# Kernel tuning notes

Measured on AMD Instinct MI355X. Metric: run time of the kernel, lower is better.

The kernel has to match this reference:

```python
import jax, jax.numpy as jnp
import numpy as np

B, MD, N = 8, 256, 4096          # batch, model_dim, n_points
H, F, S = 8, 16, 32              # heads, in_feature_dim, tensor_size (3D lattice S^3)
EPS = 1e-5


def _bn(x, g, b):
    # training-mode BatchNorm1d over (batch, points), x: [B, C, N]
    m = x.mean(axis=(0, 2), keepdims=True)
    v = x.var(axis=(0, 2), keepdims=True)
    return (x - m) * jax.lax.rsqrt(v + EPS) * g[None, :, None] + b[None, :, None]


def setup_inputs() -> dict:
    key = jax.random.key(0)
    ks = jax.random.split(key, 10)
    return {
        "x": jax.random.normal(ks[0], (B, MD, N), jnp.float32),
        "pcd": jax.random.uniform(ks[1], (B, 3, N), jnp.float32, -1.0, 1.0),
        "W_kv": jax.random.normal(ks[2], (H * (F + 3), MD), jnp.float32) / np.float32(np.sqrt(MD)),
        "key_gamma": 0.1 * jax.random.normal(ks[3], (H * 3,), jnp.float32),
        "key_beta": jnp.zeros((H * 3,), jnp.float32),
        "val_gamma": jnp.ones((H * F,), jnp.float32) + 0.1 * jax.random.normal(ks[4], (H * F,), jnp.float32),
        "val_beta": jnp.zeros((H * F,), jnp.float32),
        "R": jnp.tile(jnp.eye(3, dtype=jnp.float32), (H, 1, 1)) + 0.05 * jax.random.normal(ks[5], (H, 3, 3), jnp.float32),
        "t": 0.05 * jax.random.normal(ks[6], (H, 3), jnp.float32),
        "conv_w": jax.random.normal(ks[7], (H * F, F, 3, 3, 3), jnp.float32) / np.float32(np.sqrt(F * 27)),
        "conv_b": jnp.zeros((H * F,), jnp.float32),
        "after_gamma": jnp.ones((H * F,), jnp.float32),
        "after_beta": jnp.zeros((H * F,), jnp.float32),
    }


# precomputed 8 trilinear corner offsets
_OFFS = np.array([[dx, dy, dz] for dx in (0, 1) for dy in (0, 1) for dz in (0, 1)])
_OFF_FLAT = jnp.asarray((_OFFS[:, 0] * S + _OFFS[:, 1]) * S + _OFFS[:, 2], jnp.int32)  # [8]
_OFF_BOOL = jnp.asarray(_OFFS.astype(bool))  # [8, 3]


def _forward(x, pcd, W_kv, key_gamma, key_beta, val_gamma, val_beta, R, t,
             conv_w, conv_b, after_gamma, after_beta):
    # keys/values prediction (1x1 conv == matmul)
    kv = jnp.einsum('om,bmn->bon', W_kv, x)                      # [B, H*(F+3), N]
    keys_res = _bn(kv[:, :H * 3], key_gamma, key_beta).reshape(B, H, 3, N)
    values = _bn(kv[:, H * 3:], val_gamma, val_beta)              # [B, H*F, N]
    # per-head learned affine transform of shifted point coords (VolTransformer)
    keys = jnp.einsum('hij,bhjn->bhin', R, pcd[:, None] + keys_res) + t[None, :, :, None]
    lattice = jnp.tanh(keys)                                      # [B, H, 3, N] in (-1, 1)
    # DifferentiablePositions: map to lattice coords, split into floor index + frac
    pos = (lattice + 1.0) * 0.5 * (S - 1)
    fl_f = jnp.clip(jnp.floor(pos), 0.0, S - 2.0)
    frac = pos - fl_f                                             # differentiable local coords
    fl = fl_f.astype(jnp.int32)
    base = (fl[:, :, 0] * S + fl[:, :, 1]) * S + fl[:, :, 2]      # [B, H, N] flattened index
    idx8 = base[:, :, None, :] + _OFF_FLAT[None, None, :, None]   # [B, H, 8, N]
    # trilinear corner weights: prod_d (frac_d if corner bit else 1-frac_d)
    w8 = jnp.prod(jnp.where(_OFF_BOOL[None, None, :, :, None],
                            frac[:, :, None], 1.0 - frac[:, :, None]), axis=3)  # [B, H, 8, N]
    # Splat: weighted scatter-add onto the lattice
    vals = values.reshape(B, H, F, N)
    contrib = (vals[:, :, :, None, :] * w8[:, :, None]).reshape(B * H, F, 8 * N)
    idx_f = idx8.reshape(B * H, 8 * N)
    z = jax.vmap(lambda c, i: jnp.zeros((F, S ** 3), c.dtype).at[:, i].add(c))(contrib, idx_f)
    z = z.reshape(B, H * F, S, S, S)
    # heads-grouped 3x3x3 conv over the lattice
    zc = jax.lax.conv_general_dilated(
        z, conv_w, window_strides=(1, 1, 1), padding='SAME',
        feature_group_count=H,
        dimension_numbers=('NCDHW', 'OIDHW', 'NCDHW')) + conv_b[None, :, None, None, None]
    # Slice: gather back at the same corners with the same trilinear weights
    g = jax.vmap(lambda zf, i: zf[:, i])(zc.reshape(B * H, F, S ** 3), idx_f)  # [B*H, F, 8N]
    sliced = (g.reshape(B, H, F, 8, N) * w8[:, :, None]).sum(axis=3).reshape(B, H * F, N)
    return jax.nn.relu(_bn(sliced, after_gamma, after_beta))


def reference(x, pcd, W_kv, key_gamma, key_beta, val_gamma, val_beta, R, t,
              conv_w, conv_b, after_gamma, after_beta):
    return _forward(x, pcd, W_kv, key_gamma, key_beta, val_gamma, val_beta, R, t,
                    conv_w, conv_b, after_gamma, after_beta)
```

## Files before the change

### kernel.cpp

```cpp
#include <hip/hip_runtime.h>
#include <cstddef>
#include <cstdint>

#define BB 8
#define MD 256
#define NP 4096
#define HH 8
#define FF 16
#define SS 32
#define S3 32768
#define CC 152
#define KC 24
#define PTS (BB*HH*NP)
#define BPT (HH*NP)
#define BN_CNT (BB*NP)
#define EPSV 1e-5f
#define ZSTRH (HH*S3*FF)

typedef __attribute__((ext_vector_type(8))) short short8v;
typedef __attribute__((ext_vector_type(4))) float f32x4;

__device__ __forceinline__ unsigned int f2bf(float f) {
    unsigned int u = __float_as_uint(f);
    unsigned int r = u + 0x7FFFu + ((u >> 16) & 1u);
    return r >> 16;
}

__global__ __launch_bounds__(256) void k_wgpack(const float* __restrict__ W,
                                                unsigned short* __restrict__ wg) {
    int gid = blockIdx.x * 256 + threadIdx.x;
    if (gid >= 5120) return;
    int lane = gid & 63;
    int mc   = (gid >> 6) & 7;
    int oct  = gid >> 9;
    int oc = oct * 16 + (lane & 15);
    int m0 = mc * 32 + (lane >> 4) * 8;
    unsigned short oh[8], ol[8];
#pragma unroll
    for (int j = 0; j < 8; ++j) {
        float wv = (oc < CC) ? W[(size_t)oc * MD + m0 + j] : 0.f;
        unsigned int hi = f2bf(wv);
        float r = wv - __uint_as_float(hi << 16);
        oh[j] = (unsigned short)hi;
        ol[j] = (unsigned short)f2bf(r);
    }
    ushort4* dh = (ushort4*)(wg + (size_t)gid * 8);
    dh[0] = make_ushort4(oh[0], oh[1], oh[2], oh[3]);
    dh[1] = make_ushort4(oh[4], oh[5], oh[6], oh[7]);
    ushort4* dl = (ushort4*)(wg + (size_t)(5120 + gid) * 8);
    dl[0] = make_ushort4(ol[0], ol[1], ol[2], ol[3]);
    dl[1] = make_ushort4(ol[4], ol[5], ol[6], ol[7]);
}

__global__ __launch_bounds__(256) void k_gemm(const float* __restrict__ x,
                                              const unsigned short* __restrict__ wg,
                                              float* __restrict__ kv) {
    __shared__ __align__(16) unsigned char xh[32768];
    __shared__ __align__(16) unsigned char xlo[32768];
    int nt = blockIdx.x;
    int b  = blockIdx.y;
    int tid = threadIdx.x;
    int n_l = tid & 63, w = tid >> 6;
    int n0 = nt * 64;

    const float* xb = x + (size_t)b * MD * NP + n0;
#pragma unroll 4
    for (int k = 0; k < 32; ++k) {
        int m = k * 8 + w * 2;
        float v0 = xb[(size_t)m * NP + n_l];
        float v1 = xb[(size_t)(m + 1) * NP + n_l];
        unsigned int h0 = f2bf(v0), h1 = f2bf(v1);
        float r0 = v0 - __uint_as_float(h0 << 16);
        float r1 = v1 - __uint_as_float(h1 << 16);
        unsigned int byte = (unsigned)(n_l * 512 + m * 2) ^ (unsigned)((n_l & 7) << 4);
        *(unsigned int*)(xh + byte)  = h0 | (h1 << 16);
        *(unsigned int*)(xlo + byte) = f2bf(r0) | (f2bf(r1) << 16);
    }
    __syncthreads();

    int lane = tid & 63;
    int nn = w * 16 + (lane & 15);
    int kg = lane >> 4;
    short8v xfh[8], xfl[8];
#pragma unroll
    for (int mc = 0; mc < 8; ++mc) {
        unsigned int byte = (unsigned)(nn * 512 + (mc * 32 + kg * 8) * 2)
                          ^ (unsigned)((nn & 7) << 4);
        xfh[mc] = *(const short8v*)(xh + byte);
        xfl[mc] = *(const short8v*)(xlo + byte);
    }

    f32x4 acc[10];
#pragma unroll
    for (int t = 0; t < 10; ++t) acc[t] = (f32x4){0.f, 0.f, 0.f, 0.f};

    const short8v* wfh = (const short8v*)wg;
    const short8v* wfl = wfh + 5120;
#pragma unroll
    for (int oct = 0; oct < 10; ++oct) {
#pragma unroll
        for (int mc = 0; mc < 8; ++mc) {
            short8v wh = wfh[(oct * 8 + mc) * 64 + lane];
            short8v wl = wfl[(oct * 8 + mc) * 64 + lane];
            acc[oct] = __builtin_amdgcn_mfma_f32_16x16x32_bf16(wh, xfh[mc], acc[oct], 0, 0, 0);
            acc[oct] = __builtin_amdgcn_mfma_f32_16x16x32_bf16(wh, xfl[mc], acc[oct], 0, 0, 0);
            acc[oct] = __builtin_amdgcn_mfma_f32_16x16x32_bf16(wl, xfh[mc], acc[oct], 0, 0, 0);
        }
    }

    int n = n0 + nn;
#pragma unroll
    for (int oct = 0; oct < 10; ++oct) {
#pragma unroll
        for (int r = 0; r < 4; ++r) {
            int oc = oct * 16 + kg * 4 + r;
            if (oc < CC)
                kv[((size_t)b * CC + oc) * NP + n] = acc[oct][r];
        }
    }
}

__global__ __launch_bounds__(256) void k_stats_kv(const float* __restrict__ kv,
                                                  const float* __restrict__ kg,
                                                  const float* __restrict__ kb,
                                                  const float* __restrict__ vg,
                                                  const float* __restrict__ vb,
                                                  float* __restrict__ A,
                                                  float* __restrict__ Bv) {
    int o = blockIdx.x, tid = threadIdx.x;
    float s = 0.f, ss = 0.f;
    for (int b = 0; b < BB; ++b) {
        const float* p = kv + ((size_t)b * CC + o) * NP;
        for (int n = tid; n < NP; n += 256) { float v = p[n]; s += v; ss = fmaf(v, v, ss); }
    }
#pragma unroll
    for (int off = 32; off > 0; off >>= 1) { s += __shfl_down(s, off); ss += __shfl_down(ss, off); }
    __shared__ float sh[8];
    int lane = tid & 63, w = tid >> 6;
    if (lane == 0) { sh[w] = s; sh[4 + w] = ss; }
    __syncthreads();
    if (tid == 0) {
        float S_ = sh[0] + sh[1] + sh[2] + sh[3];
        float SSv = sh[4] + sh[5] + sh[6] + sh[7];
        float mean = S_ * (1.f / BN_CNT);
        float var  = SSv * (1.f / BN_CNT) - mean * mean;
        float rstd = rsqrtf(var + EPSV);
        float g  = (o < KC) ? kg[o] : vg[o - KC];
        float be = (o < KC) ? kb[o] : vb[o - KC];
        A[o]  = rstd * g;
        Bv[o] = be - mean * rstd * g;
    }
}

__global__ __launch_bounds__(256) void k_prep(const float* __restrict__ kv,
                                              const float* __restrict__ pcd,
                                              const float* __restrict__ A,
                                              const float* __restrict__ Bv,
                                              const float* __restrict__ R,
                                              const float* __restrict__ t,
                                              int* __restrict__ base,
                                              float* __restrict__ frac,
                                              float* __restrict__ vals) {
    int gid = blockIdx.x * 256 + threadIdx.x;
    int b = gid >> 15, h = (gid >> 12) & 7, n = gid & 4095;

    float p[3];
#pragma unroll
    for (int i = 0; i < 3; ++i) {
        int c = h * 3 + i;
        float v = kv[((size_t)b * CC + c) * NP + n];
        p[i] = pcd[((size_t)b * 3 + i) * NP + n] + fmaf(A[c], v, Bv[c]);
    }
    int fl[3]; float fr[3];
#pragma unroll
    for (int i = 0; i < 3; ++i) {
        float key = R[h * 9 + i * 3 + 0] * p[0] + R[h * 9 + i * 3 + 1] * p[1] +
                    R[h * 9 + i * 3 + 2] * p[2] + t[h * 3 + i];
        float lat = tanhf(key);
        float pos = (lat + 1.f) * 0.5f * (SS - 1);
        float flf = fminf(fmaxf(floorf(pos), 0.f), (float)(SS - 2));
        fr[i] = pos - flf;
        fl[i] = (int)flf;
    }
    base[gid] = (fl[0] * SS + fl[1]) * SS + fl[2];
    frac[gid]           = fr[0];
    frac[PTS + gid]     = fr[1];
    frac[2 * PTS + gid] = fr[2];

    float4* vo = (float4*)(vals + (size_t)gid * 16);
#pragma unroll
    for (int q = 0; q < 4; ++q) {
        float4 v;
        float* vv = (float*)&v;
#pragma unroll
        for (int j = 0; j < 4; ++j) {
            int c = KC + h * FF + q * 4 + j;
            vv[j] = fmaf(A[c], kv[((size_t)b * CC + c) * NP + n], Bv[c]);
        }
        vo[q] = v;
    }
}

__global__ __launch_bounds__(256) void k_bin(const int* __restrict__ base,
                                             const float* __restrict__ frac,
                                             int4* __restrict__ sorted,
                                             int* __restrict__ bin_start) {
    __shared__ int hist[1024];
    __shared__ int curs[1024];
    int bh = blockIdx.x;
    int tid = threadIdx.x;
    for (int k = tid; k < 1024; k += 256) hist[k] = 0;
    __syncthreads();
    int gb = bh * NP;
    for (int p = tid; p < NP; p += 256)
        atomicAdd(&hist[base[gb + p] >> 5], 1);
    __syncthreads();
    if (tid == 0) {
        int run = 0;
        for (int k = 0; k < 1024; ++k) { int c = hist[k]; hist[k] = run; run += c; }
    }
    __syncthreads();
    for (int k = tid; k < 1024; k += 256) {
        bin_start[bh * 1024 + k] = hist[k];
        curs[k] = hist[k];
    }
    __syncthreads();
    for (int p = tid; p < NP; p += 256) {
        int bs = base[gb + p];
        int slot = atomicAdd(&curs[bs >> 5], 1);
        sorted[(size_t)bh * NP + slot] =
            make_int4(p | (bs << 12),
                      __float_as_int(frac[gb + p]),
                      __float_as_int(frac[PTS + gb + p]),
                      __float_as_int(frac[2 * PTS + gb + p]));
    }
}

__global__ __launch_bounds__(256) void k_vperm(const int4* __restrict__ sorted,
                                               const float* __restrict__ vals,
                                               unsigned short* __restrict__ vals_s) {
    int gid = blockIdx.x * 256 + threadIdx.x;
    int j = gid >> 1, half = gid & 1;
    int bh = j >> 12;
    int p = sorted[j].x & 4095;
    const float4* src = (const float4*)(vals + ((size_t)bh * NP + p) * 16) + half * 2;
    float4 a = src[0], c = src[1];
    uint4 o;
    o.x = f2bf(a.x) | (f2bf(a.y) << 16);
    o.y = f2bf(a.z) | (f2bf(a.w) << 16);
    o.z = f2bf(c.x) | (f2bf(c.y) << 16);
    o.w = f2bf(c.z) | (f2bf(c.w) << 16);
    *(uint4*)(vals_s + (size_t)j * 16 + half * 8) = o;
}

__global__ __launch_bounds__(256) void k_wpack(const float* __restrict__ cw,
                                               unsigned short* __restrict__ wApack) {
    int gid = blockIdx.x * 256 + threadIdx.x;
    if (gid >= 8 * 14 * 64) return;
    int lane = gid & 63;
    int m = (gid >> 6) % 14;
    int h = gid / (14 * 64);
    int fo = lane & 15, g = lane >> 4;
    int tap = 2 * m + (g >> 1);
    int ci0 = (g & 1) * 8;
    unsigned short o[8];
#pragma unroll
    for (int j = 0; j < 8; ++j) {
        float w = (tap <= 26) ? cw[((size_t)(h * 16 + fo) * 16 + ci0 + j) * 27 + tap] : 0.f;
        o[j] = (unsigned short)f2bf(w);
    }
    ushort4* dst = (ushort4*)(wApack + (size_t)gid * 8);
    dst[0] = make_ushort4(o[0], o[1], o[2], o[3]);
    dst[1] = make_ushort4(o[4], o[5], o[6], o[7]);
}

__global__ __launch_bounds__(64) void k_splat(const int4* __restrict__ sorted,
                                              const int* __restrict__ bin_start,
                                              const unsigned short* __restrict__ vsrc,
                                              unsigned short* __restrict__ zout,
                                              int b0) {
    __shared__ float zl[4][32][16];
    int x  = blockIdx.x;
    int yq = blockIdx.y;
    int hq = blockIdx.z;
    int h = hq & 7, bq = hq >> 3;
    int bh = (b0 + bq) * 8 + h;
    int lane = threadIdx.x;
    int ch = lane & 15, cor = lane >> 4;
    int dyb = cor >> 1, dzb = cor & 1;
    int row_lo = yq * 4;
    int ylo = row_lo - 1; if (ylo < 0) ylo = 0;
    int yhi = row_lo + 4;

    float4* zl4 = (float4*)zl;
    float4 zero4 = make_float4(0.f, 0.f, 0.f, 0.f);
    for (int i = lane; i < 512; i += 64) zl4[i] = zero4;
    __syncthreads();

    const int4* srt = sorted + (size_t)bh * NP;
    const unsigned short* vb = vsrc + (size_t)bh * NP * 16;
    const int* bsrt = bin_start + bh * 1024;
    int yzoff = dyb * 32 + dzb - row_lo * 32;

#pragma unroll
    for (int pass = 0; pass < 2; ++pass) {
        int s = x - 1 + pass;
        if (s < 0 || s > 30) continue;
        int j0 = bsrt[s * 32 + ylo];
        int j1 = bsrt[s * 32 + yhi];
        bool dxh = (pass == 0);
        for (int j = j0; j < j1; j += 8) {
            int4 rec[8];
            float v[8];
#pragma unroll
            for (int u = 0; u < 8; ++u) {
                int jc = j + u; jc = (jc < NP - 1) ? jc : (NP - 1);
                rec[u] = srt[jc];
            }
#pragma unroll
            for (int u = 0; u < 8; ++u) {
                int jc = j + u; jc = (jc < NP - 1) ? jc : (NP - 1);
                v[u] = __uint_as_float((unsigned)vb[(size_t)jc * 16 + ch] << 16);
            }
#pragma unroll
            for (int u = 0; u < 8; ++u) {
                int bs = rec[u].x >> 12;
                int r = ((bs >> 5) & 31) + dyb;
                if (j + u < j1 && (unsigned)(r - row_lo) < 4u) {
                    float fx = __int_as_float(rec[u].y);
                    float fy = __int_as_float(rec[u].z);
                    float fz = __int_as_float(rec[u].w);
                    float w = (dxh ? fx : 1.f - fx) * (dyb ? fy : 1.f - fy) *
                              (dzb ? fz : 1.f - fz);
                    int addr = (bs & 1023) + yzoff;
                    (&zl[0][0][0])[addr * 16 + ch] += w * v[u];
                }
            }
        }
    }
    __syncthreads();

    for (int i = lane; i < 256; i += 64) {
        int cl = i >> 1, half = i & 1;
        float4 a = zl4[cl * 4 + half * 2];
        float4 c = zl4[cl * 4 + half * 2 + 1];
        uint4 o;
        o.x = f2bf(a.x) | (f2bf(a.y) << 16);
        o.y = f2bf(a.z) | (f2bf(a.w) << 16);
        o.z = f2bf(c.x) | (f2bf(c.y) << 16);
        o.w = f2bf(c.z) | (f2bf(c.w) << 16);
        int gcell = x * 1024 + row_lo * 32 + cl;
        *(uint4*)&zout[((size_t)(bq * HH + h) * S3 + gcell) * 16 + half * 8] = o;
    }
}

__global__ __launch_bounds__(256) void k_conv(const unsigned short* __restrict__ z,
                                              const unsigned short* __restrict__ wApack,
                                              const float* __restrict__ cb,
                                              unsigned short* __restrict__ zc) {
    __shared__ __align__(16) unsigned short zl[4][10][34][16];
    int bx = blockIdx.x;
    int yq = blockIdx.y;
    int gz = blockIdx.z;
    int h  = gz & 7;
    int bq = gz >> 3;
    int tid = threadIdx.x;
    int lane = tid & 63, wid = tid >> 6;
    int x2 = bx * 2;

    const unsigned short* zb = z + (size_t)bq * ZSTRH;
    unsigned short* zcb = zc + (size_t)bq * ZSTRH;

    short8v af[14];
    const short8v* wa = (const short8v*)(wApack + (size_t)h * 14 * 64 * 8);
#pragma unroll
    for (int m = 0; m < 14; ++m) af[m] = wa[m * 64 + lane];

    for (int i = tid; i < 4 * 10 * 34; i += 256) {
        int dxi = i / 340, rem = i % 340;
        int yy = rem / 34, zi = rem % 34;
        int gx = x2 + dxi - 1, gy = yq * 8 + yy - 1, gzz = zi - 1;
        uint4* d4 = (uint4*)(&zl[0][0][0][0] + (size_t)i * 16);
        if (gx >= 0 && gx < SS && gy >= 0 && gy < SS && gzz >= 0 && gzz < SS) {
            const uint4* src = (const uint4*)&zb[((size_t)h * S3 +
                                 (gx * 1024 + gy * 32 + gzz)) * 16];
            d4[0] = src[0];
            d4[1] = src[1];
        } else {
            uint4 zz4 = make_uint4(0, 0, 0, 0);
            d4[0] = zz4; d4[1] = zz4;
        }
    }
    __syncthreads();

    bool lo = (lane & 32) == 0;
    int ci0 = (lane & 16) ? 8 : 0;
    int l15 = lane & 15;
    int fo0 = (lane >> 4) * 4;
    float4 bias = *(const float4*)&cb[h * 16 + fo0];
    const unsigned short* zlf = &zl[0][0][0][0];

#pragma unroll 1
    for (int i = 0; i < 8; ++i) {
        int gi = wid * 8 + i;
        int xl = gi >> 4, yl = (gi >> 1) & 7, zz0 = (gi & 1) * 16;
        int invbase = xl * 340 + yl * 34 + zz0 + l15;

        f32x4 acc = {0.f, 0.f, 0.f, 0.f};
#pragma unroll
        for (int m = 0; m < 14; ++m) {
            const int t0 = 2 * m;
            const int t1 = (2 * m + 1 > 26) ? 26 : (2 * m + 1);
            const int off0 = (t0 / 9) * 340 + ((t0 % 9) / 3) * 34 + (t0 % 3);
            const int off1 = (t1 / 9) * 340 + ((t1 % 9) / 3) * 34 + (t1 % 3);
            int offc = lo ? off0 : off1;
            const short8v* bp = (const short8v*)(zlf + (size_t)(invbase + offc) * 16 + ci0);
            acc = __builtin_amdgcn_mfma_f32_16x16x32_bf16(af[m], *bp, acc, 0, 0, 0);
        }
        int cell = (x2 + xl) * 1024 + (yq * 8 + yl) * 32 + zz0 + l15;
        uint2 o;
        o.x = f2bf(acc[0] + bias.x) | (f2bf(acc[1] + bias.y) << 16);
        o.y = f2bf(acc[2] + bias.z) | (f2bf(acc[3] + bias.w) << 16);
        *(uint2*)&zcb[((size_t)h * S3 + cell) * 16 + fo0] = o;
    }
}

__global__ __launch_bounds__(256) void k_slice(const int* __restrict__ base,
                                               const float* __restrict__ frac,
                                               const unsigned short* __restrict__ zc,
                                               float* __restrict__ out, int b0) {
    int lid = blockIdx.x * 256 + threadIdx.x;
    int bq = blockIdx.y;
    int b = b0 + bq;
    int h = lid >> 12, n = lid & 4095;
    int gid = b * BPT + lid;
    int bs = base[gid];
    float fx = frac[gid], fy = frac[PTS + gid], fz = frac[2 * PTS + gid];
    float wx[2] = {1.f - fx, fx}, wy[2] = {1.f - fy, fy}, wz[2] = {1.f - fz, fz};
    const unsigned short* zb = zc + (size_t)bq * ZSTRH + (size_t)h * S3 * FF;

    float acc[16];
#pragma unroll
    for (int f = 0; f < 16; ++f) acc[f] = 0.f;
#pragma unroll
    for (int dx = 0; dx < 2; ++dx)
#pragma unroll
    for (int dy = 0; dy < 2; ++dy)
#pragma unroll
    for (int dz = 0; dz < 2; ++dz) {
        int cell = bs + dx * (SS * SS) + dy * SS + dz;
        float w = wx[dx] * wy[dy] * wz[dz];
        const uint4* src = (const uint4*)&zb[(size_t)cell * 16];
        uint4 u0 = src[0];
        uint4 u1 = src[1];
        acc[0]  = fmaf(__uint_as_float(u0.x << 16), w, acc[0]);
        acc[1]  = fmaf(__uint_as_float(u0.x & 0xffff0000u), w, acc[1]);
        acc[2]  = fmaf(__uint_as_float(u0.y << 16), w, acc[2]);
        acc[3]  = fmaf(__uint_as_float(u0.y & 0xffff0000u), w, acc[3]);
        acc[4]  = fmaf(__uint_as_float(u0.z << 16), w, acc[4]);
        acc[5]  = fmaf(__uint_as_float(u0.z & 0xffff0000u), w, acc[5]);
        acc[6]  = fmaf(__uint_as_float(u0.w << 16), w, acc[6]);
        acc[7]  = fmaf(__uint_as_float(u0.w & 0xffff0000u), w, acc[7]);
        acc[8]  = fmaf(__uint_as_float(u1.x << 16), w, acc[8]);
        acc[9]  = fmaf(__uint_as_float(u1.x & 0xffff0000u), w, acc[9]);
        acc[10] = fmaf(__uint_as_float(u1.y << 16), w, acc[10]);
        acc[11] = fmaf(__uint_as_float(u1.y & 0xffff0000u), w, acc[11]);
        acc[12] = fmaf(__uint_as_float(u1.z << 16), w, acc[12]);
        acc[13] = fmaf(__uint_as_float(u1.z & 0xffff0000u), w, acc[13]);
        acc[14] = fmaf(__uint_as_float(u1.w << 16), w, acc[14]);
        acc[15] = fmaf(__uint_as_float(u1.w & 0xffff0000u), w, acc[15]);
    }
    size_t ob = ((size_t)b * (HH * FF) + h * FF) * NP + n;
#pragma unroll
    for (int f = 0; f < 16; ++f)
        out[ob + (size_t)f * NP] = acc[f];
}

__global__ __launch_bounds__(256) void k_stats2(const float* __restrict__ out,
                                                const float* __restrict__ ag,
                                                const float* __restrict__ ab,
                                                float* __restrict__ A2,
                                                float* __restrict__ B2) {
    int c = blockIdx.x, tid = threadIdx.x;
    float s = 0.f, ss = 0.f;
    for (int b = 0; b < BB; ++b) {
        const float* p = out + ((size_t)b * (HH * FF) + c) * NP;
        for (int n = tid; n < NP; n += 256) { float v = p[n]; s += v; ss = fmaf(v, v, ss); }
    }
#pragma unroll
    for (int off = 32; off > 0; off >>= 1) { s += __shfl_down(s, off); ss += __shfl_down(ss, off); }
    __shared__ float sh[8];
    int lane = tid & 63, w = tid >> 6;
    if (lane == 0) { sh[w] = s; sh[4 + w] = ss; }
    __syncthreads();
    if (tid == 0) {
        float S_ = sh[0] + sh[1] + sh[2] + sh[3];
        float SSv = sh[4] + sh[5] + sh[6] + sh[7];
        float mean = S_ * (1.f / BN_CNT);
        float var  = SSv * (1.f / BN_CNT) - mean * mean;
        float rstd = rsqrtf(var + EPSV);
        A2[c] = rstd * ag[c];
        B2[c] = ab[c] - mean * rstd * ag[c];
    }
}

__global__ __launch_bounds__(256) void k_bnrelu(float* __restrict__ out,
                                                const float* __restrict__ A2,
                                                const float* __restrict__ B2) {
    int gid = blockIdx.x * 256 + threadIdx.x;
    int c = (gid >> 12) & 127;
    float v = out[gid];
    out[gid] = fmaxf(fmaf(A2[c], v, B2[c]), 0.f);
}

extern "C" void kernel_launch(void* const* d_in, const int* in_sizes, int n_in,
                              void* d_out, int out_size, void* d_ws, size_t ws_size,
                              hipStream_t stream) {
    (void)in_sizes; (void)n_in; (void)out_size;
    const float* x   = (const float*)d_in[0];
    const float* pcd = (const float*)d_in[1];
    const float* W   = (const float*)d_in[2];
    const float* kg  = (const float*)d_in[3];
    const float* kb  = (const float*)d_in[4];
    const float* vg  = (const float*)d_in[5];
    const float* vb  = (const float*)d_in[6];
    const float* R   = (const float*)d_in[7];
    const float* t   = (const float*)d_in[8];
    const float* cw  = (const float*)d_in[9];
    const float* cb  = (const float*)d_in[10];
    const float* ag  = (const float*)d_in[11];
    const float* ab  = (const float*)d_in[12];
    float* out = (float*)d_out;
    char* ws = (char*)d_ws;

    float* kv   = (float*)(ws + 0);
    int4*  sorted    = (int4*)(ws + 8388608ULL);
    int*   bin_start = (int*) (ws + 12582912ULL);
    unsigned short* wApack = (unsigned short*)(ws + 16777216ULL);
    int*   base = (int*)  (ws + 19922944ULL);
    float* frac = (float*)(ws + 20971520ULL);
    float* A    = (float*)(ws + 24117248ULL);
    float* Bv   = (float*)(ws + 24118272ULL);
    float* A2   = (float*)(ws + 24119296ULL);
    float* B2   = (float*)(ws + 24120320ULL);
    float* vals = (float*)(ws + 24121344ULL);

    int NB = 1;
    if (ws_size >= 40898560ULL + 8ULL * 16777216ULL + 8388608ULL)      NB = 8;
    else if (ws_size >= 40898560ULL + 4ULL * 16777216ULL + 8388608ULL) NB = 4;
    else if (ws_size >= 40898560ULL + 2ULL * 16777216ULL + 8388608ULL) NB = 2;

    unsigned short* z_bf;
    unsigned short* zc;
    unsigned short* vals_s;
    if (NB == 1) {
        z_bf = (unsigned short*)kv;
        zc   = (unsigned short*)(ws + 40898560ULL);
        vals_s = (unsigned short*)(ws + 49287168ULL);
    } else {
        z_bf = (unsigned short*)(ws + 40898560ULL);
        zc   = (unsigned short*)(ws + 40898560ULL + (size_t)NB * 8388608ULL);
        vals_s = (unsigned short*)(ws + 40898560ULL + (size_t)NB * 16777216ULL);
    }
    unsigned short* wg = (unsigned short*)zc;

    k_wgpack<<<dim3(20), 256, 0, stream>>>(W, wg);
    k_gemm<<<dim3(64, BB), 256, 0, stream>>>(x, wg, kv);
    k_stats_kv<<<dim3(CC), 256, 0, stream>>>(kv, kg, kb, vg, vb, A, Bv);
    k_prep<<<dim3(PTS / 256), 256, 0, stream>>>(kv, pcd, A, Bv, R, t, base, frac, vals);
    k_bin<<<dim3(BB * HH), 256, 0, stream>>>(base, frac, sorted, bin_start);
    k_vperm<<<dim3(PTS * 2 / 256), 256, 0, stream>>>(sorted, vals, vals_s);
    k_wpack<<<dim3(28), 256, 0, stream>>>(cw, wApack);

    for (int b0 = 0; b0 < BB; b0 += NB) {
        k_splat<<<dim3(SS, 8, HH * NB), 64, 0, stream>>>(sorted, bin_start, vals_s,
                                                         z_bf, b0);
        k_conv<<<dim3(16, 4, HH * NB), 256, 0, stream>>>(z_bf, wApack, cb, zc);
        k_slice<<<dim3(BPT / 256, NB), 256, 0, stream>>>(base, frac, zc, out, b0);
    }

    k_stats2<<<dim3(HH * FF), 256, 0, stream>>>(out, ag, ab, A2, B2);
    k_bnrelu<<<dim3((BB * HH * FF * NP) / 256), 256, 0, stream>>>(out, A2, B2);
}
```

Measured before the change: 303.6 us.

## Fuse bf16 value permutation into binning and fold output BN stats into slice

k_prep now writes values directly as bf16, and k_bin copies each point's value row into sorted order, which removes the separate k_vperm pass and halves the value intermediate. k_slice now reduces per-channel sum and sum-of-squares through wave shuffles and global atomics, replacing the separate k_stats2 pass that re-read the whole output. The costs are 16-way shuffle reductions with atomics in every slice block, a tiny zeroing kernel, and a value copy done by only 64 blocks in k_bin. Accumulating with float atomics also makes the stats order-dependent.

```diff
diff --git a/kernel.cpp b/kernel.cpp
--- a/kernel.cpp
+++ b/kernel.cpp
@@ -160,7 +160,7 @@
                                               const float* __restrict__ t,
                                               int* __restrict__ base,
                                               float* __restrict__ frac,
-                                              float* __restrict__ vals) {
+                                              unsigned short* __restrict__ vals) {
     int gid = blockIdx.x * 256 + threadIdx.x;
     int b = gid >> 15, h = (gid >> 12) & 7, n = gid & 4095;
 
@@ -187,24 +187,30 @@
     frac[PTS + gid]     = fr[1];
     frac[2 * PTS + gid] = fr[2];
 
-    float4* vo = (float4*)(vals + (size_t)gid * 16);
-#pragma unroll
-    for (int q = 0; q < 4; ++q) {
-        float4 v;
-        float* vv = (float*)&v;
-#pragma unroll
-        for (int j = 0; j < 4; ++j) {
-            int c = KC + h * FF + q * 4 + j;
-            vv[j] = fmaf(A[c], kv[((size_t)b * CC + c) * NP + n], Bv[c]);
-        }
-        vo[q] = v;
+    float vv[16];
+#pragma unroll
+    for (int f = 0; f < 16; ++f) {
+        int c = KC + h * FF + f;
+        vv[f] = fmaf(A[c], kv[((size_t)b * CC + c) * NP + n], Bv[c]);
+    }
+    uint4* vo = (uint4*)(vals + (size_t)gid * 16);
+#pragma unroll
+    for (int q = 0; q < 2; ++q) {
+        uint4 o;
+        o.x = f2bf(vv[q * 8 + 0]) | (f2bf(vv[q * 8 + 1]) << 16);
+        o.y = f2bf(vv[q * 8 + 2]) | (f2bf(vv[q * 8 + 3]) << 16);
+        o.z = f2bf(vv[q * 8 + 4]) | (f2bf(vv[q * 8 + 5]) << 16);
+        o.w = f2bf(vv[q * 8 + 6]) | (f2bf(vv[q * 8 + 7]) << 16);
+        vo[q] = o;
     }
 }
 
 __global__ __launch_bounds__(256) void k_bin(const int* __restrict__ base,
                                              const float* __restrict__ frac,
+                                             const unsigned short* __restrict__ vals,
                                              int4* __restrict__ sorted,
-                                             int* __restrict__ bin_start) {
+                                             int* __restrict__ bin_start,
+                                             unsigned short* __restrict__ vals_s) {
     __shared__ int hist[1024];
     __shared__ int curs[1024];
     int bh = blockIdx.x;
@@ -233,24 +239,11 @@
                       __float_as_int(frac[gb + p]),
                       __float_as_int(frac[PTS + gb + p]),
                       __float_as_int(frac[2 * PTS + gb + p]));
-    }
-}
-
-__global__ __launch_bounds__(256) void k_vperm(const int4* __restrict__ sorted,
-                                               const float* __restrict__ vals,
-                                               unsigned short* __restrict__ vals_s) {
-    int gid = blockIdx.x * 256 + threadIdx.x;
-    int j = gid >> 1, half = gid & 1;
-    int bh = j >> 12;
-    int p = sorted[j].x & 4095;
-    const float4* src = (const float4*)(vals + ((size_t)bh * NP + p) * 16) + half * 2;
-    float4 a = src[0], c = src[1];
-    uint4 o;
-    o.x = f2bf(a.x) | (f2bf(a.y) << 16);
-    o.y = f2bf(a.z) | (f2bf(a.w) << 16);
-    o.z = f2bf(c.x) | (f2bf(c.y) << 16);
-    o.w = f2bf(c.z) | (f2bf(c.w) << 16);
-    *(uint4*)(vals_s + (size_t)j * 16 + half * 8) = o;
+        const uint4* vsrc = (const uint4*)(vals + (size_t)(gb + p) * 16);
+        uint4* vdst = (uint4*)(vals_s + ((size_t)bh * NP + slot) * 16);
+        vdst[0] = vsrc[0];
+        vdst[1] = vsrc[1];
+    }
 }
 
 __global__ __launch_bounds__(256) void k_wpack(const float* __restrict__ cw,
@@ -272,6 +265,10 @@
     ushort4* dst = (ushort4*)(wApack + (size_t)gid * 8);
     dst[0] = make_ushort4(o[0], o[1], o[2], o[3]);
     dst[1] = make_ushort4(o[4], o[5], o[6], o[7]);
+}
+
+__global__ __launch_bounds__(256) void k_zero(float* __restrict__ sums) {
+    sums[threadIdx.x] = 0.f;
 }
 
 __global__ __launch_bounds__(64) void k_splat(const int4* __restrict__ sorted,
@@ -428,10 +425,14 @@
 __global__ __launch_bounds__(256) void k_slice(const int* __restrict__ base,
                                                const float* __restrict__ frac,
                                                const unsigned short* __restrict__ zc,
-                                               float* __restrict__ out, int b0) {
+                                               float* __restrict__ out,
+                                               float* __restrict__ sums, int b0) {
+    __shared__ float shs[4][16];
+    __shared__ float shq[4][16];
     int lid = blockIdx.x * 256 + threadIdx.x;
     int bq = blockIdx.y;
     int b = b0 + bq;
+    int tid = threadIdx.x;
     int h = lid >> 12, n = lid & 4095;
     int gid = b * BPT + lid;
     int bs = base[gid];
@@ -474,34 +475,45 @@
 #pragma unroll
     for (int f = 0; f < 16; ++f)
         out[ob + (size_t)f * NP] = acc[f];
-}
-
-__global__ __launch_bounds__(256) void k_stats2(const float* __restrict__ out,
-                                                const float* __restrict__ ag,
-                                                const float* __restrict__ ab,
-                                                float* __restrict__ A2,
-                                                float* __restrict__ B2) {
-    int c = blockIdx.x, tid = threadIdx.x;
-    float s = 0.f, ss = 0.f;
-    for (int b = 0; b < BB; ++b) {
-        const float* p = out + ((size_t)b * (HH * FF) + c) * NP;
-        for (int n = tid; n < NP; n += 256) { float v = p[n]; s += v; ss = fmaf(v, v, ss); }
-    }
-#pragma unroll
-    for (int off = 32; off > 0; off >>= 1) { s += __shfl_down(s, off); ss += __shfl_down(ss, off); }
-    __shared__ float sh[8];
-    int lane = tid & 63, w = tid >> 6;
-    if (lane == 0) { sh[w] = s; sh[4 + w] = ss; }
-    __syncthreads();
-    if (tid == 0) {
-        float S_ = sh[0] + sh[1] + sh[2] + sh[3];
-        float SSv = sh[4] + sh[5] + sh[6] + sh[7];
-        float mean = S_ * (1.f / BN_CNT);
-        float var  = SSv * (1.f / BN_CNT) - mean * mean;
-        float rstd = rsqrtf(var + EPSV);
-        A2[c] = rstd * ag[c];
-        B2[c] = ab[c] - mean * rstd * ag[c];
-    }
+
+    float s[16], q[16];
+#pragma unroll
+    for (int f = 0; f < 16; ++f) { s[f] = acc[f]; q[f] = acc[f] * acc[f]; }
+#pragma unroll
+    for (int off = 32; off > 0; off >>= 1) {
+#pragma unroll
+        for (int f = 0; f < 16; ++f) {
+            s[f] += __shfl_down(s[f], off);
+            q[f] += __shfl_down(q[f], off);
+        }
+    }
+    int lane = tid & 63, wid = tid >> 6;
+    if (lane == 0) {
+#pragma unroll
+        for (int f = 0; f < 16; ++f) { shs[wid][f] = s[f]; shq[wid][f] = q[f]; }
+    }
+    __syncthreads();
+    if (tid < 16) {
+        float S = shs[0][tid] + shs[1][tid] + shs[2][tid] + shs[3][tid];
+        atomicAdd(&sums[h * 16 + tid], S);
+    } else if (tid < 32) {
+        int f = tid - 16;
+        float Q = shq[0][f] + shq[1][f] + shq[2][f] + shq[3][f];
+        atomicAdd(&sums[128 + h * 16 + f], Q);
+    }
+}
+
+__global__ __launch_bounds__(128) void k_stats2fin(const float* __restrict__ sums,
+                                                   const float* __restrict__ ag,
+                                                   const float* __restrict__ ab,
+                                                   float* __restrict__ A2,
+                                                   float* __restrict__ B2) {
+    int c = threadIdx.x;
+    float mean = sums[c] * (1.f / BN_CNT);
+    float var  = sums[128 + c] * (1.f / BN_CNT) - mean * mean;
+    float rstd = rsqrtf(var + EPSV);
+    A2[c] = rstd * ag[c];
+    B2[c] = ab[c] - mean * rstd * ag[c];
 }
 
 __global__ __launch_bounds__(256) void k_bnrelu(float* __restrict__ out,
@@ -543,7 +555,8 @@
     float* Bv   = (float*)(ws + 24118272ULL);
     float* A2   = (float*)(ws + 24119296ULL);
     float* B2   = (float*)(ws + 24120320ULL);
-    float* vals = (float*)(ws + 24121344ULL);
+    unsigned short* vals = (unsigned short*)(ws + 24121344ULL);
+    float* sums = (float*)(ws + 32509952ULL);
 
     int NB = 1;
     if (ws_size >= 40898560ULL + 8ULL * 16777216ULL + 8388608ULL)      NB = 8;
@@ -568,17 +581,17 @@
     k_gemm<<<dim3(64, BB), 256, 0, stream>>>(x, wg, kv);
     k_stats_kv<<<dim3(CC), 256, 0, stream>>>(kv, kg, kb, vg, vb, A, Bv);
     k_prep<<<dim3(PTS / 256), 256, 0, stream>>>(kv, pcd, A, Bv, R, t, base, frac, vals);
-    k_bin<<<dim3(BB * HH), 256, 0, stream>>>(base, frac, sorted, bin_start);
-    k_vperm<<<dim3(PTS * 2 / 256), 256, 0, stream>>>(sorted, vals, vals_s);
+    k_bin<<<dim3(BB * HH), 256, 0, stream>>>(base, frac, vals, sorted, bin_start, vals_s);
     k_wpack<<<dim3(28), 256, 0, stream>>>(cw, wApack);
+    k_zero<<<dim3(1), 256, 0, stream>>>(sums);
 
     for (int b0 = 0; b0 < BB; b0 += NB) {
         k_splat<<<dim3(SS, 8, HH * NB), 64, 0, stream>>>(sorted, bin_start, vals_s,
                                                          z_bf, b0);
         k_conv<<<dim3(16, 4, HH * NB), 256, 0, stream>>>(z_bf, wApack, cb, zc);
-        k_slice<<<dim3(BPT / 256, NB), 256, 0, stream>>>(base, frac, zc, out, b0);
-    }
-
-    k_stats2<<<dim3(HH * FF), 256, 0, stream>>>(out, ag, ab, A2, B2);
+        k_slice<<<dim3(BPT / 256, NB), 256, 0, stream>>>(base, frac, zc, out, sums, b0);
+    }
+
+    k_stats2fin<<<dim3(1), 128, 0, stream>>>(sums, ag, ab, A2, B2);
     k_bnrelu<<<dim3((BB * HH * FF * NP) / 256), 256, 0, stream>>>(out, A2, B2);
 }
```

After: 263.1 us (median of 2 runs). 13.4% less time.
